# Kernel optimization log

Measured on AMD Instinct MI355X. Metric: run time of the kernel, lower is better.

## Reference

```python
import jax, jax.numpy as jnp
import numpy as np

B, T, D, H = 2, 2048, 1024, 16
HD = D // H  # head dim = 64


def setup_inputs() -> dict:
    key = jax.random.key(0)
    ks = jax.random.split(key, 8)
    scale = 0.02
    return {
        "query_states": jax.random.normal(ks[0], (B, T, D), jnp.float32),
        "key_states": jax.random.normal(ks[1], (B, T, D), jnp.float32),
        "query_mask": jnp.ones((B, T), jnp.float32),
        "key_mask": jnp.ones((B, T), jnp.float32),
        "Wq": jax.random.normal(ks[2], (D, D), jnp.float32) * scale,
        "bq": jnp.zeros((D,), jnp.float32),
        "Wk": jax.random.normal(ks[3], (D, D), jnp.float32) * scale,
        "bk": jnp.zeros((D,), jnp.float32),
        "Wv": jax.random.normal(ks[4], (D, D), jnp.float32) * scale,
        "bv": jnp.zeros((D,), jnp.float32),
        "mask_future": 1,
    }


def _split_heads(x):  # [B,T,D] -> [B,H,T,HD]
    return x.reshape(B, T, H, HD).transpose(0, 2, 1, 3)


def reference(query_states, key_states, query_mask, key_mask, Wq, bq, Wk, bk, Wv, bv, mask_future):
    q = _split_heads(query_states @ Wq.T + bq)
    k = _split_heads(key_states @ Wk.T + bk)
    v = _split_heads(key_states @ Wv.T + bv)
    # [B,H,T,T]
    scores = jnp.einsum("bhqd,bhkd->bhqk", q, k) / jnp.sqrt(jnp.float32(HD))
    scores = scores + (1.0 - key_mask)[:, None, None, :] * -10000.0
    if mask_future:
        causal = (1.0 - jnp.tril(jnp.ones((T, T), jnp.float32))) * -10000.0
        scores = scores + causal[None, None, :, :]
    probs = jax.nn.softmax(scores, axis=-1)
    probs = probs * query_mask[:, None, :, None]  # post-softmax query mask
    ctx = jnp.einsum("bhqk,bhkd->bhqd", probs, v)
    return ctx.transpose(0, 2, 1, 3).reshape(B, T, D)
```

## Files before the change

kernel.cpp:

```cpp
#include <hip/hip_runtime.h>
#include <hip/hip_bf16.h>
#include <stdint.h>

typedef __attribute__((ext_vector_type(8))) short short8;
typedef __attribute__((ext_vector_type(4))) short short4_t;
typedef __attribute__((ext_vector_type(4))) float f32x4;

#define B_ 2
#define T_ 2048
#define D_ 1024
#define H_ 16
#define HD_ 64
#define BT_ 4096
#define NKT64 32

__device__ __forceinline__ unsigned short f2bf(float f) {
    union { float f; uint32_t u; } v; v.f = f;
    uint32_t u = v.u;
    uint32_t r = (u + 0x7fffu + ((u >> 16) & 1u)) >> 16;
    return (unsigned short)r;
}

__device__ __forceinline__ uint32_t pack2(float a, float b) {
    return (uint32_t)f2bf(a) | ((uint32_t)f2bf(b) << 16);
}

__device__ __forceinline__ void gld16(const void* g, void* l) {
    __builtin_amdgcn_global_load_lds((const __attribute__((address_space(1))) void*)g,
                                     (__attribute__((address_space(3))) void*)l, 16, 0, 0);
}

__device__ __forceinline__ int swz(int x) { return x ^ (((x >> 7) & 7) << 4); }

__global__ __launch_bounds__(256) void cvt2(const float* __restrict__ s0, unsigned short* __restrict__ d0,
                                            const float* __restrict__ s1, unsigned short* __restrict__ d1,
                                            const float* __restrict__ kmask, float* __restrict__ kpen_g,
                                            int n8) {
    int i = blockIdx.x * 256 + threadIdx.x;
    if (blockIdx.y == 2) {
        if (i < B_ * T_) kpen_g[i] = (1.0f - kmask[i]) * -10000.0f;
        return;
    }
    const float* src = blockIdx.y ? s1 : s0;
    unsigned short* dst = blockIdx.y ? d1 : d0;
    if (i >= n8) return;
    const float4* s = (const float4*)src + (size_t)i * 2;
    float4 a = s[0], b4 = s[1];
    short8 o;
    o[0] = (short)f2bf(a.x);  o[1] = (short)f2bf(a.y);
    o[2] = (short)f2bf(a.z);  o[3] = (short)f2bf(a.w);
    o[4] = (short)f2bf(b4.x); o[5] = (short)f2bf(b4.y);
    o[6] = (short)f2bf(b4.z); o[7] = (short)f2bf(b4.w);
    *(short8*)(dst + (size_t)i * 8) = o;
}

__global__ __launch_bounds__(256) void cvt3(const float* __restrict__ s0, unsigned short* __restrict__ d0,
                                            const float* __restrict__ s1, unsigned short* __restrict__ d1,
                                            const float* __restrict__ s2, unsigned short* __restrict__ d2,
                                            int n8) {
    const float* src = blockIdx.y == 0 ? s0 : (blockIdx.y == 1 ? s1 : s2);
    unsigned short* dst = blockIdx.y == 0 ? d0 : (blockIdx.y == 1 ? d1 : d2);
    int i = blockIdx.x * 256 + threadIdx.x;
    if (i >= n8) return;
    const float4* s = (const float4*)src + (size_t)i * 2;
    float4 a = s[0], b4 = s[1];
    short8 o;
    o[0] = (short)f2bf(a.x);  o[1] = (short)f2bf(a.y);
    o[2] = (short)f2bf(a.z);  o[3] = (short)f2bf(a.w);
    o[4] = (short)f2bf(b4.x); o[5] = (short)f2bf(b4.y);
    o[6] = (short)f2bf(b4.z); o[7] = (short)f2bf(b4.w);
    *(short8*)(dst + (size_t)i * 8) = o;
}

__global__ __launch_bounds__(256) void qkv_gemm_fused(const unsigned short* __restrict__ xq,
                                                      const unsigned short* __restrict__ xk,
                                                      const unsigned short* __restrict__ wq,
                                                      const unsigned short* __restrict__ wk,
                                                      const unsigned short* __restrict__ wv,
                                                      const float* __restrict__ bq,
                                                      const float* __restrict__ bk,
                                                      const float* __restrict__ bv,
                                                      unsigned short* __restrict__ q_ws,
                                                      unsigned short* __restrict__ k_ws,
                                                      unsigned short* __restrict__ v8_ws) {
    __shared__ unsigned short Al[128 * 32];
    __shared__ unsigned short Bl[128 * 32];
    const int K = D_;
    int z = blockIdx.z;
    const unsigned short* X = (z == 0) ? xq : xk;
    const unsigned short* W = (z == 0) ? wq : (z == 1 ? wk : wv);
    const float* bias = (z == 0) ? bq : (z == 1 ? bk : bv);

    int m0 = blockIdx.x * 128, n0 = blockIdx.y * 128;
    int tid = threadIdx.x, lane = tid & 63, w = tid >> 6;
    int wr = w >> 1, wc = w & 1;

    f32x4 acc[4][4];
#pragma unroll
    for (int i = 0; i < 4; i++)
#pragma unroll
        for (int j = 0; j < 4; j++) acc[i][j] = (f32x4){0.f, 0.f, 0.f, 0.f};

    int srow0 = (lane >> 2);
    int skch = (lane & 3) * 8;

    for (int kt = 0; kt < K / 32; ++kt) {
        int kb = kt * 32;
#pragma unroll
        for (int t = 0; t < 2; ++t) {
            int ins = w * 2 + t;
            int row = ins * 16 + srow0;
            gld16(X + (size_t)(m0 + row) * K + kb + skch, (char*)Al + ins * 1024);
            gld16(W + (size_t)(n0 + row) * K + kb + skch, (char*)Bl + ins * 1024);
        }
        __syncthreads();
        short8 af[4], bf[4];
#pragma unroll
        for (int mi = 0; mi < 4; mi++)
            af[mi] = *(const short8*)(Al + (wr * 64 + mi * 16 + (lane & 15)) * 32 + (lane >> 4) * 8);
#pragma unroll
        for (int ni = 0; ni < 4; ni++)
            bf[ni] = *(const short8*)(Bl + (wc * 64 + ni * 16 + (lane & 15)) * 32 + (lane >> 4) * 8);
#pragma unroll
        for (int mi = 0; mi < 4; mi++)
#pragma unroll
            for (int ni = 0; ni < 4; ni++)
                acc[mi][ni] = __builtin_amdgcn_mfma_f32_16x16x32_bf16(af[mi], bf[ni], acc[mi][ni], 0, 0, 0);
        __syncthreads();
    }

    if (z < 2) {
        unsigned short* outp = (z == 0) ? q_ws : k_ws;
#pragma unroll
        for (int ni = 0; ni < 4; ni++) {
            int n = n0 + wc * 64 + ni * 16 + (lane & 15);
            float bv2 = bias[n];
            int h = n >> 6, hd = n & 63;
#pragma unroll
            for (int mi = 0; mi < 4; mi++) {
#pragma unroll
                for (int r = 0; r < 4; r++) {
                    int m = m0 + wr * 64 + mi * 16 + (lane >> 4) * 4 + r;
                    int b = m >> 11, t = m & (T_ - 1);
                    outp[((size_t)(b * H_ + h) * T_ + t) * HD_ + hd] = f2bf(acc[mi][ni][r] + bv2);
                }
            }
        }
    } else {
#pragma unroll
        for (int ni = 0; ni < 4; ni++) {
            int n = n0 + wc * 64 + ni * 16 + (lane & 15);
            float bv2 = bias[n];
            int h = n >> 6, hd = n & 63;
#pragma unroll
            for (int mi = 0; mi < 4; mi++) {
                int m = m0 + wr * 64 + mi * 16 + (lane >> 4) * 4;
                int b = m >> 11, t = m & (T_ - 1);
                short4_t pk;
#pragma unroll
                for (int r = 0; r < 4; r++) pk[r] = (short)f2bf(acc[mi][ni][r] + bv2);
                *(short4_t*)(v8_ws + (((size_t)(b * H_ + h) * 256 + (t >> 3)) * HD_ + hd) * 8 + (t & 7)) = pk;
            }
        }
    }
}

__global__ __launch_bounds__(128, 2) void attn(const unsigned short* __restrict__ q_ws,
                                               const unsigned short* __restrict__ k_ws,
                                               const unsigned short* __restrict__ v8_ws,
                                               const float* __restrict__ qmask,
                                               const float* __restrict__ kpen_g,
                                               const int* __restrict__ mfp,
                                               float* __restrict__ out) {
    __shared__ char Pl[2 * 2 * 2048];

    int w = threadIdx.x >> 6;
    int lane = threadIdx.x & 63;
    int lg = lane >> 4, q = lane & 15;
    int wid = blockIdx.x * 2 + w;
    int qt = 63 - (wid >> 5);
    int bh = wid & 31;
    int b = bh >> 4, h = bh & 15;
    int q0 = qt * 32;
    int mf = mfp[0];
    int nkt = mf ? (qt >> 1) + 1 : NKT64;
    char* Pw = Pl + w * 4096;

    short8 qf[2][2];
#pragma unroll
    for (int m = 0; m < 2; m++) {
        const unsigned short* qp = q_ws + ((size_t)bh * T_ + q0 + m * 16 + q) * HD_ + lg * 8;
        qf[m][0] = *(const short8*)qp;
        qf[m][1] = *(const short8*)(qp + 32);
    }

    f32x4 o[2][4];
#pragma unroll
    for (int m = 0; m < 2; m++)
#pragma unroll
        for (int i = 0; i < 4; i++) o[m][i] = (f32x4){0.f, 0.f, 0.f, 0.f};
    float mrow[2] = {-1e30f, -1e30f};
    float lrow[2] = {0.f, 0.f};

    const float* kpenb = kpen_g + b * T_;

    auto loadK = [&](int kv0, short8 (&ka)[4], short8 (&kb)[4]) {
#pragma unroll
        for (int nb = 0; nb < 4; nb++) {
            const unsigned short* kp = k_ws + ((size_t)bh * T_ + kv0 + nb * 16 + q) * HD_ + lg * 8;
            ka[nb] = *(const short8*)kp;
            kb[nb] = *(const short8*)(kp + 32);
        }
    };

    auto tile_step = [&](int kv0, const short8 (&ka)[4], const short8 (&kb)[4]) {
        f32x4 s[2][4];
        __builtin_amdgcn_s_setprio(1);
#pragma unroll
        for (int nb = 0; nb < 4; nb++) {
#pragma unroll
            for (int m = 0; m < 2; m++) {
                f32x4 z = (f32x4){0.f, 0.f, 0.f, 0.f};
                z = __builtin_amdgcn_mfma_f32_16x16x32_bf16(ka[nb], qf[m][0], z, 0, 0, 0);
                z = __builtin_amdgcn_mfma_f32_16x16x32_bf16(kb[nb], qf[m][1], z, 0, 0, 0);
                s[m][nb] = z;
            }
        }
        __builtin_amdgcn_s_setprio(0);

        short8 vf[4][2];
        const unsigned short* vbase = v8_ws + (((size_t)bh * 256 + (kv0 >> 3) + lg) * 64 + q) * 8;
#pragma unroll
        for (int nbh = 0; nbh < 4; nbh++) {
            vf[nbh][0] = *(const short8*)(vbase + nbh * 128);
            vf[nbh][1] = *(const short8*)(vbase + nbh * 128 + 2048);
        }

        f32x4 kp4[4];
#pragma unroll
        for (int nb = 0; nb < 4; nb++)
            kp4[nb] = *(const f32x4*)(kpenb + kv0 + nb * 16 + lg * 4);

        bool diag = mf && (kv0 + 63 > q0);
        float sc[2];
#pragma unroll
        for (int m = 0; m < 2; m++) {
            int qg = q0 + m * 16 + q;
#pragma unroll
            for (int nb = 0; nb < 4; nb++) {
#pragma unroll
                for (int r = 0; r < 4; r++) {
                    float v = s[m][nb][r] * 0.125f + kp4[nb][r];
                    if (diag) {
                        int kvg = kv0 + nb * 16 + lg * 4 + r;
                        v = (kvg > qg) ? v - 10000.0f : v;
                    }
                    s[m][nb][r] = v;
                }
            }
            float xm = fmaxf(
                fmaxf(fmaxf(fmaxf(s[m][0][0], s[m][0][1]), fmaxf(s[m][0][2], s[m][0][3])),
                      fmaxf(fmaxf(s[m][1][0], s[m][1][1]), fmaxf(s[m][1][2], s[m][1][3]))),
                fmaxf(fmaxf(fmaxf(s[m][2][0], s[m][2][1]), fmaxf(s[m][2][2], s[m][2][3])),
                      fmaxf(fmaxf(s[m][3][0], s[m][3][1]), fmaxf(s[m][3][2], s[m][3][3]))));
            xm = fmaxf(xm, __shfl_xor(xm, 16));
            xm = fmaxf(xm, __shfl_xor(xm, 32));
            float mn = fmaxf(mrow[m], xm);
            sc[m] = __expf(mrow[m] - mn);
            mrow[m] = mn;

#pragma unroll
            for (int nb = 0; nb < 4; nb++)
#pragma unroll
                for (int r = 0; r < 4; r++) s[m][nb][r] = __expf(s[m][nb][r] - mn);

            float rs = ((s[m][0][0] + s[m][0][1]) + (s[m][0][2] + s[m][0][3]))
                     + ((s[m][1][0] + s[m][1][1]) + (s[m][1][2] + s[m][1][3]))
                     + ((s[m][2][0] + s[m][2][1]) + (s[m][2][2] + s[m][2][3]))
                     + ((s[m][3][0] + s[m][3][1]) + (s[m][3][2] + s[m][3][3]));
            rs += __shfl_xor(rs, 16);
            rs += __shfl_xor(rs, 32);
            lrow[m] = lrow[m] * sc[m] + rs;

#pragma unroll
            for (int nbh = 0; nbh < 4; nbh++)
#pragma unroll
                for (int r = 0; r < 4; r++) o[m][nbh][r] *= sc[m];

#pragma unroll
            for (int nb = 0; nb < 4; nb++) {
                uint2 ww;
                ww.x = pack2(s[m][nb][0], s[m][nb][1]);
                ww.y = pack2(s[m][nb][2], s[m][nb][3]);
                *(uint2*)(Pw + m * 2048 + swz(q * 128 + nb * 32 + lg * 8)) = ww;
            }
        }

        short8 pf[2][2];
#pragma unroll
        for (int m = 0; m < 2; m++) {
            pf[m][0] = *(const short8*)(Pw + m * 2048 + swz(q * 128 + lg * 16));
            pf[m][1] = *(const short8*)(Pw + m * 2048 + swz(q * 128 + 64 + lg * 16));
        }

        __builtin_amdgcn_s_setprio(1);
#pragma unroll
        for (int nbh = 0; nbh < 4; nbh++) {
#pragma unroll
            for (int m = 0; m < 2; m++) {
                o[m][nbh] = __builtin_amdgcn_mfma_f32_16x16x32_bf16(vf[nbh][0], pf[m][0], o[m][nbh], 0, 0, 0);
                o[m][nbh] = __builtin_amdgcn_mfma_f32_16x16x32_bf16(vf[nbh][1], pf[m][1], o[m][nbh], 0, 0, 0);
            }
        }
        __builtin_amdgcn_s_setprio(0);
    };

    short8 kA0[4], kA1[4], kB0[4], kB1[4];
    loadK(0, kA0, kA1);
    int kt = 0;
    while (true) {
        int kvn = (kt + 1 < nkt ? kt + 1 : kt) * 64;
        loadK(kvn, kB0, kB1);
        tile_step(kt * 64, kA0, kA1);
        if (++kt >= nkt) break;
        int kvn2 = (kt + 1 < nkt ? kt + 1 : kt) * 64;
        loadK(kvn2, kA0, kA1);
        tile_step(kt * 64, kB0, kB1);
        if (++kt >= nkt) break;
    }

#pragma unroll
    for (int m = 0; m < 2; m++) {
        int qg = q0 + m * 16 + q;
        float inv = qmask[b * T_ + qg] / lrow[m];
        float* op = out + ((size_t)(b * T_ + qg)) * D_ + h * 64 + lg * 4;
#pragma unroll
        for (int nbh = 0; nbh < 4; nbh++) {
            f32x4 ov;
#pragma unroll
            for (int r = 0; r < 4; r++) ov[r] = o[m][nbh][r] * inv;
            *(f32x4*)(op + nbh * 16) = ov;
        }
    }
}

extern "C" void kernel_launch(void* const* d_in, const int* in_sizes, int n_in,
                              void* d_out, int out_size, void* d_ws, size_t ws_size,
                              hipStream_t stream) {
    const float* xq = (const float*)d_in[0];
    const float* xk = (const float*)d_in[1];
    const float* qmask = (const float*)d_in[2];
    const float* kmask = (const float*)d_in[3];
    const float* Wq = (const float*)d_in[4];
    const float* bq = (const float*)d_in[5];
    const float* Wk = (const float*)d_in[6];
    const float* bk = (const float*)d_in[7];
    const float* Wv = (const float*)d_in[8];
    const float* bv = (const float*)d_in[9];
    const int* mf = (const int*)d_in[10];
    float* out = (float*)d_out;

    char* ws = (char*)d_ws;
    unsigned short* xq_bf = (unsigned short*)(ws);
    unsigned short* xk_bf = (unsigned short*)(ws + (8u << 20));
    unsigned short* wq_bf = (unsigned short*)(ws + (16u << 20));
    unsigned short* wk_bf = (unsigned short*)(ws + (18u << 20));
    unsigned short* wv_bf = (unsigned short*)(ws + (20u << 20));
    unsigned short* q_ws  = (unsigned short*)(ws + (22u << 20));
    unsigned short* k_ws  = (unsigned short*)(ws + (30u << 20));
    unsigned short* v8_ws = (unsigned short*)(ws + (38u << 20));
    float* kpen_g         = (float*)(ws + (46u << 20));

    cvt2<<<dim3(BT_ * D_ / 8 / 256, 3), 256, 0, stream>>>(xq, xq_bf, xk, xk_bf, kmask, kpen_g, BT_ * D_ / 8);
    cvt3<<<dim3(D_ * D_ / 8 / 256, 3), 256, 0, stream>>>(Wq, wq_bf, Wk, wk_bf, Wv, wv_bf, D_ * D_ / 8);

    dim3 gg(BT_ / 128, D_ / 128, 3);
    qkv_gemm_fused<<<gg, 256, 0, stream>>>(xq_bf, xk_bf, wq_bf, wk_bf, wv_bf, bq, bk, bv,
                                           q_ws, k_ws, v8_ws);

    attn<<<1024, 128, 0, stream>>>(q_ws, k_ws, v8_ws, qmask, kpen_g, mf, out);
}
```

Baseline: 137.0 us.

## Split KV tiles across four waves per query tile and merge partials in LDS

Each attention block now holds four waves that share one query tile and head. Each wave processes a contiguous slice of the KV tiles, then the per-wave partial outputs and softmax max/sum statistics are written to shared memory and merged with rescaling. The aim is more parallelism and shorter per-wave critical paths, especially for long causal rows. The cost is extra LDS traffic, a block barrier and idle waves on short causal rows. The merge assumes the row max is stored in the natural-exp domain.

After: 171.5 us. +25.1%, slower.

```diff
diff --git a/kernel.cpp b/kernel.cpp
--- a/kernel.cpp
+++ b/kernel.cpp
@@ -165,26 +165,32 @@
     }
 }
 
-__global__ __launch_bounds__(128, 2) void attn(const unsigned short* __restrict__ q_ws,
+__global__ __launch_bounds__(256, 3) void attn(const unsigned short* __restrict__ q_ws,
                                                const unsigned short* __restrict__ k_ws,
                                                const unsigned short* __restrict__ v8_ws,
                                                const float* __restrict__ qmask,
                                                const float* __restrict__ kpen_g,
                                                const int* __restrict__ mfp,
                                                float* __restrict__ out) {
-    __shared__ char Pl[2 * 2 * 2048];
+    __shared__ char Pl[4 * 4096];
+    __shared__ float OS[4 * 2048];
+    __shared__ float ML[4 * 2 * 16 * 2];
 
     int w = threadIdx.x >> 6;
     int lane = threadIdx.x & 63;
     int lg = lane >> 4, q = lane & 15;
-    int wid = blockIdx.x * 2 + w;
-    int qt = 63 - (wid >> 5);
-    int bh = wid & 31;
+    int bid = blockIdx.x;
+    int qt = 63 - (bid >> 5);
+    int bh = bid & 31;
     int b = bh >> 4, h = bh & 15;
     int q0 = qt * 32;
     int mf = mfp[0];
     int nkt = mf ? (qt >> 1) + 1 : NKT64;
     char* Pw = Pl + w * 4096;
+
+    int base = nkt >> 2, rem = nkt & 3;
+    int cnt = base + (w < rem ? 1 : 0);
+    int start = w * base + (w < rem ? w : rem);
 
     short8 qf[2][2];
 #pragma unroll
@@ -315,32 +321,60 @@
         __builtin_amdgcn_s_setprio(0);
     };
 
-    short8 kA0[4], kA1[4], kB0[4], kB1[4];
-    loadK(0, kA0, kA1);
-    int kt = 0;
-    while (true) {
-        int kvn = (kt + 1 < nkt ? kt + 1 : kt) * 64;
-        loadK(kvn, kB0, kB1);
-        tile_step(kt * 64, kA0, kA1);
-        if (++kt >= nkt) break;
-        int kvn2 = (kt + 1 < nkt ? kt + 1 : kt) * 64;
-        loadK(kvn2, kA0, kA1);
-        tile_step(kt * 64, kB0, kB1);
-        if (++kt >= nkt) break;
-    }
+    if (cnt > 0) {
+        short8 kA0[4], kA1[4], kB0[4], kB1[4];
+        int c1 = start + cnt;
+        loadK(start * 64, kA0, kA1);
+        int kt = start;
+        while (true) {
+            int kvn = (kt + 1 < c1 ? kt + 1 : kt) * 64;
+            loadK(kvn, kB0, kB1);
+            tile_step(kt * 64, kA0, kA1);
+            if (++kt >= c1) break;
+            kvn = (kt + 1 < c1 ? kt + 1 : kt) * 64;
+            loadK(kvn, kA0, kA1);
+            tile_step(kt * 64, kB0, kB1);
+            if (++kt >= c1) break;
+        }
+    }
+
+#pragma unroll
+    for (int m = 0; m < 2; m++)
+#pragma unroll
+        for (int nbh = 0; nbh < 4; nbh++)
+            *(f32x4*)(OS + w * 2048 + ((m * 4 + nbh) * 64 + lane) * 4) = o[m][nbh];
+    if (lane < 16) {
+#pragma unroll
+        for (int m = 0; m < 2; m++) {
+            float2 ml2 = make_float2(mrow[m], lrow[m]);
+            *(float2*)(ML + ((w * 2 + m) * 16 + q) * 2) = ml2;
+        }
+    }
+    __syncthreads();
 
 #pragma unroll
     for (int m = 0; m < 2; m++) {
+        float2 ml0 = *(const float2*)(ML + ((0 * 2 + m) * 16 + q) * 2);
+        float2 ml1 = *(const float2*)(ML + ((1 * 2 + m) * 16 + q) * 2);
+        float2 ml2 = *(const float2*)(ML + ((2 * 2 + m) * 16 + q) * 2);
+        float2 ml3 = *(const float2*)(ML + ((3 * 2 + m) * 16 + q) * 2);
+        float M = fmaxf(fmaxf(ml0.x, ml1.x), fmaxf(ml2.x, ml3.x));
+        float e0 = __expf(ml0.x - M), e1 = __expf(ml1.x - M);
+        float e2 = __expf(ml2.x - M), e3 = __expf(ml3.x - M);
+        float den = ml0.y * e0 + ml1.y * e1 + ml2.y * e2 + ml3.y * e3;
+
+        f32x4 O0 = *(const f32x4*)(OS + 0 * 2048 + ((m * 4 + w) * 64 + lane) * 4);
+        f32x4 O1 = *(const f32x4*)(OS + 1 * 2048 + ((m * 4 + w) * 64 + lane) * 4);
+        f32x4 O2 = *(const f32x4*)(OS + 2 * 2048 + ((m * 4 + w) * 64 + lane) * 4);
+        f32x4 O3 = *(const f32x4*)(OS + 3 * 2048 + ((m * 4 + w) * 64 + lane) * 4);
+
         int qg = q0 + m * 16 + q;
-        float inv = qmask[b * T_ + qg] / lrow[m];
-        float* op = out + ((size_t)(b * T_ + qg)) * D_ + h * 64 + lg * 4;
-#pragma unroll
-        for (int nbh = 0; nbh < 4; nbh++) {
-            f32x4 ov;
-#pragma unroll
-            for (int r = 0; r < 4; r++) ov[r] = o[m][nbh][r] * inv;
-            *(f32x4*)(op + nbh * 16) = ov;
-        }
+        float inv = qmask[b * T_ + qg] / den;
+        f32x4 ov;
+#pragma unroll
+        for (int r = 0; r < 4; r++)
+            ov[r] = (O0[r] * e0 + O1[r] * e1 + O2[r] * e2 + O3[r] * e3) * inv;
+        *(f32x4*)(out + ((size_t)(b * T_ + qg)) * D_ + h * 64 + w * 16 + lg * 4) = ov;
     }
 }
 
@@ -378,5 +412,5 @@
     qkv_gemm_fused<<<gg, 256, 0, stream>>>(xq_bf, xk_bf, wq_bf, wk_bf, wv_bf, bq, bk, bv,
                                            q_ws, k_ws, v8_ws);
 
-    attn<<<1024, 128, 0, stream>>>(q_ws, k_ws, v8_ws, qmask, kpen_g, mf, out);
-}
+    attn<<<2048, 256, 0, stream>>>(q_ws, k_ws, v8_ws, qmask, kpen_g, mf, out);
+}
```
